# Kernel optimization log

Hardware: AMD Instinct MI355X
Metric: run time of the kernel (lower is better)

The kernel has to match this reference:

```python
import jax, jax.numpy as jnp
import numpy as np


def setup_inputs() -> dict:
    key = jax.random.key(0)
    ks = jax.random.split(key, 7)
    B, T, E, H = 4, 4096, 1024, 64
    return {
        "idx": jax.random.normal(ks[0], (B, T, E), dtype=jnp.float32),
        "Wq": jax.random.normal(ks[1], (E, H), dtype=jnp.float32) * (E ** -0.5),
        "bq": jax.random.normal(ks[2], (H,), dtype=jnp.float32) * 0.01,
        "Wk": jax.random.normal(ks[3], (E, H), dtype=jnp.float32) * (E ** -0.5),
        "bk": jax.random.normal(ks[4], (H,), dtype=jnp.float32) * 0.01,
        "Wv": jax.random.normal(ks[5], (E, H), dtype=jnp.float32) * (E ** -0.5),
        "bv": jax.random.normal(ks[6], (H,), dtype=jnp.float32) * 0.01,
    }


def reference(idx, Wq, bq, Wk, bk, Wv, bv):
    # idx: [B, T, E]
    d = idx.shape[-1]  # note: torch code scales by n_embd**-0.5, NOT head_size
    Q = idx @ Wq + bq  # [B, T, H]
    K = idx @ Wk + bk
    V = idx @ Wv + bv
    # scores; NOTE: original torch code calls wei.masked_fill(...) non-in-place
    # and discards the result, so no causal mask is applied. No softmax either.
    wei = jnp.einsum("bth,bsh->bts", Q, K) * (d ** -0.5)  # [B, T, T]
    out = jnp.einsum("bts,bsh->bth", wei, V)  # [B, T, H]
    return out
```

## Files before the change

### kernel.cpp

```cpp
#include <hip/hip_runtime.h>


typedef __attribute__((ext_vector_type(8))) short bf16x8;
typedef __attribute__((ext_vector_type(4))) float f32x4;

#define MFMA16(a, b, c) __builtin_amdgcn_mfma_f32_16x16x32_bf16((a), (b), (c), 0, 0, 0)

__device__ __forceinline__ unsigned short f2bf(float f) {
    unsigned int u = __float_as_uint(f);
    u += 0x7fffu + ((u >> 16) & 1u);
    return (unsigned short)(u >> 16);
}

__global__ void prep(const float* __restrict__ Wq, const float* __restrict__ Wk,
                     const float* __restrict__ Wv, unsigned short* __restrict__ WB,
                     float* __restrict__ Mf) {
    int t = blockIdx.x * 256 + threadIdx.x;
    if (t < 16384) Mf[t] = 0.f;
    int kki = t / 768;
    int rem = t - kki * 768;
    int nt = rem >> 6, lane = rem & 63;
    int n = nt * 16 + (lane & 15);
    int kb = kki * 32 + ((lane >> 4) * 8);
    int mm = n >> 6, h = n & 63;
    const float* W = (mm == 0) ? Wq : (mm == 1) ? Wk : Wv;
    float sc = (mm == 1) ? 0.03125f : 1.0f;
    bf16x8 v;
    #pragma unroll
    for (int j = 0; j < 8; j++) v[j] = (short)f2bf(W[(size_t)(kb + j) * 64 + h] * sc);
    *(bf16x8*)(WB + (size_t)t * 8) = v;
}

__global__ __launch_bounds__(256, 2) void qkv_m(
    const float* __restrict__ idx, const unsigned short* __restrict__ WB,
    const float* __restrict__ bq, const float* __restrict__ bk, const float* __restrict__ bv,
    unsigned short* __restrict__ Q, float* __restrict__ Mf) {
    __shared__ unsigned short As[32 * 1032];
    __shared__ unsigned short Lq[32 * 68];
    unsigned short* Lk = As;
    unsigned short* Lv = As + 64 * 36;

    const int tid = threadIdx.x, lane = tid & 63, w = tid >> 6;
    const int r0 = blockIdx.x * 32;

    {
        const float* src = idx + (size_t)(r0 + w * 8) * 1024;
        #pragma unroll
        for (int batch = 0; batch < 4; batch++) {
            float4 v[8];
            #pragma unroll
            for (int j = 0; j < 8; j++)
                v[j] = *(const float4*)(src + (size_t)(batch * 8 + j) * 256 + lane * 4);
            #pragma unroll
            for (int j = 0; j < 8; j++) {
                int i   = batch * 8 + j;
                int row = w * 8 + (i >> 2);
                int k   = (i & 3) * 256 + lane * 4;
                unsigned int lo = ((unsigned int)f2bf(v[j].y) << 16) | f2bf(v[j].x);
                unsigned int hi = ((unsigned int)f2bf(v[j].w) << 16) | f2bf(v[j].z);
                uint2 p; p.x = lo; p.y = hi;
                *(uint2*)(As + (size_t)row * 1032 + k) = p;
            }
        }
    }
    __syncthreads();

    const f32x4 z4 = {0.f, 0.f, 0.f, 0.f};
    f32x4 acc[2][3] = {{z4, z4, z4}, {z4, z4, z4}};
    {
        const unsigned short* a_base0 = As + (size_t)(lane & 15) * 1032 + ((lane >> 4) * 8);
        const unsigned short* a_base1 = a_base0 + 16 * 1032;
        bf16x8 a_c[2], b0[3], b1[3], b2[3];
        a_c[0] = *(const bf16x8*)a_base0;
        a_c[1] = *(const bf16x8*)a_base1;
        {
            const unsigned short* Bp0 = WB + (size_t)(lane * 8);
            const unsigned short* Bp1 = WB + (size_t)(12 * 64 + lane) * 8;
            #pragma unroll
            for (int j = 0; j < 3; j++) {
                b0[j] = *(const bf16x8*)(Bp0 + (w + j * 4) * 512);
                b1[j] = *(const bf16x8*)(Bp1 + (w + j * 4) * 512);
                b2[j] = b1[j];
            }
        }
        for (int kk = 0; kk < 32; kk++) {
            bf16x8 na0 = a_c[0], na1 = a_c[1];
            if (kk < 30) {
                const unsigned short* Bp = WB + (size_t)(((kk + 2) * 12) * 64 + lane) * 8;
                #pragma unroll
                for (int j = 0; j < 3; j++) b2[j] = *(const bf16x8*)(Bp + (w + j * 4) * 512);
            }
            if (kk < 31) {
                na0 = *(const bf16x8*)(a_base0 + (kk + 1) * 32);
                na1 = *(const bf16x8*)(a_base1 + (kk + 1) * 32);
            }
            #pragma unroll
            for (int j = 0; j < 3; j++) {
                acc[0][j] = MFMA16(a_c[0], b0[j], acc[0][j]);
                acc[1][j] = MFMA16(a_c[1], b0[j], acc[1][j]);
            }
            #pragma unroll
            for (int j = 0; j < 3; j++) { b0[j] = b1[j]; b1[j] = b2[j]; }
            a_c[0] = na0; a_c[1] = na1;
        }
    }

    __syncthreads();
    {
        const int h     = w * 16 + (lane & 15);
        const int rbase = (lane >> 4) * 4;
        float bias0 = bq[h], bias1 = bk[h] * 0.03125f, bias2 = bv[h];
        #pragma unroll
        for (int rf = 0; rf < 2; rf++) {
            #pragma unroll
            for (int reg = 0; reg < 4; reg++) {
                int r = rf * 16 + rbase + reg;
                Lq[r * 68 + h] = f2bf(acc[rf][0][reg] + bias0);
                Lk[h * 36 + r] = f2bf(acc[rf][1][reg] + bias1);
                Lv[h * 36 + r] = f2bf(acc[rf][2][reg] + bias2);
            }
        }
    }
    __syncthreads();

    {
        int qr = tid >> 3, qh = (tid & 7) * 8;
        *(uint4*)(Q + (size_t)(r0 + qr) * 64 + qh) = *(const uint4*)(Lq + qr * 68 + qh);
    }

    {
        const int tq = (lane >> 4) * 8;
        bf16x8 a = *(const bf16x8*)&Lk[(16 * w + (lane & 15)) * 36 + tq];
        f32x4 accM[4];
        #pragma unroll
        for (int nt = 0; nt < 4; nt++) {
            bf16x8 bb = *(const bf16x8*)&Lv[(nt * 16 + (lane & 15)) * 36 + tq];
            accM[nt] = MFMA16(a, bb, z4);
        }
        float* P = Mf + (size_t)(r0 >> 12) * 4096;
        const int rowb = 16 * w + (lane >> 4) * 4;
        #pragma unroll
        for (int nt = 0; nt < 4; nt++)
            #pragma unroll
            for (int reg = 0; reg < 4; reg++)
                atomicAdd(&P[(rowb + reg) * 64 + nt * 16 + (lane & 15)], accM[nt][reg]);
    }
}

__global__ __launch_bounds__(256) void qm(
    const unsigned short* __restrict__ Q, const float* __restrict__ Mf,
    float* __restrict__ out) {
    __shared__ unsigned short Lm[64 * 72];
    const int lane = threadIdx.x & 63, wave = threadIdx.x >> 6;
    const int r0 = blockIdx.x * 64;
    const int b  = r0 >> 12;
    {
        const int tt = threadIdx.x;
        int h1 = tt >> 2, h2c = (tt & 3) * 16;
        const float* Mp = Mf + (size_t)b * 4096 + h1 * 64 + h2c;
        float vals[16];
        *(float4*)(vals + 0)  = *(const float4*)(Mp + 0);
        *(float4*)(vals + 4)  = *(const float4*)(Mp + 4);
        *(float4*)(vals + 8)  = *(const float4*)(Mp + 8);
        *(float4*)(vals + 12) = *(const float4*)(Mp + 12);
        #pragma unroll
        for (int u = 0; u < 16; u++) Lm[(h2c + u) * 72 + h1] = f2bf(vals[u]);
    }
    __syncthreads();
    const f32x4 z4 = {0.f, 0.f, 0.f, 0.f};
    f32x4 acc[4] = {z4, z4, z4, z4};
    const int rr = r0 + 16 * wave + (lane & 15);
    const int kq = (lane >> 4) * 8;
    #pragma unroll
    for (int ks = 0; ks < 2; ks++) {
        int k0 = ks * 32;
        bf16x8 a = *(const bf16x8*)&Q[(size_t)rr * 64 + k0 + kq];
        #pragma unroll
        for (int nt = 0; nt < 4; nt++) {
            bf16x8 bb = *(const bf16x8*)&Lm[(size_t)(nt * 16 + (lane & 15)) * 72 + k0 + kq];
            acc[nt] = MFMA16(a, bb, acc[nt]);
        }
    }
    const int rowb = r0 + 16 * wave + (lane >> 4) * 4;
    #pragma unroll
    for (int nt = 0; nt < 4; nt++)
        #pragma unroll
        for (int reg = 0; reg < 4; reg++)
            out[(size_t)(rowb + reg) * 64 + nt * 16 + (lane & 15)] = acc[nt][reg];
}

extern "C" void kernel_launch(void* const* d_in, const int* in_sizes, int n_in,
                              void* d_out, int out_size, void* d_ws, size_t ws_size,
                              hipStream_t stream) {
    const float* idx = (const float*)d_in[0];
    const float* Wq  = (const float*)d_in[1];
    const float* bq  = (const float*)d_in[2];
    const float* Wk  = (const float*)d_in[3];
    const float* bk  = (const float*)d_in[4];
    const float* Wv  = (const float*)d_in[5];
    const float* bv  = (const float*)d_in[6];
    float* out = (float*)d_out;

    char* ws = (char*)d_ws;
    unsigned short* WB = (unsigned short*)(ws);
    float*          Mf = (float*)(ws + (1024u << 10));
    unsigned short* Q  = (unsigned short*)(ws + (2048u << 10));

    hipLaunchKernelGGL(prep,  dim3(96),  dim3(256), 0, stream, Wq, Wk, Wv, WB, Mf);
    hipLaunchKernelGGL(qkv_m, dim3(512), dim3(256), 0, stream,
                       idx, WB, bq, bk, bv, Q, Mf);
    hipLaunchKernelGGL(qm,    dim3(256), dim3(256), 0, stream, Q, Mf, out);
}
```

Before: 123.5 us.

## Stream A tiles straight from global and spread atomic reductions over partial buffers

The QKV projection kernel no longer stages the full 32x1024 input tile in shared memory. Each lane now loads its fp32 MFMA operand fragments directly from global memory, converts them with packed bf16 conversion instructions, and double-buffers them alongside the weight fragments. This frees about 66KB of LDS per block, so the launch bounds are raised to allow three blocks per CU. The K^T·V atomic accumulation is split across 8 partial copies chosen by block index to reduce contention on the same addresses, and the final kernel sums the 8 partials. The costs are that A loads are less coalesced, which relies on the cache, and the extra partial buffers must be zeroed and read.

```diff
diff --git a/kernel.cpp b/kernel.cpp
--- a/kernel.cpp
+++ b/kernel.cpp
@@ -12,11 +12,26 @@
     return (unsigned short)(u >> 16);
 }
 
+__device__ __forceinline__ unsigned int cvtpk(float a, float b) {
+    unsigned int r;
+    asm("v_cvt_pk_bf16_f32 %0, %1, %2" : "=v"(r) : "v"(a), "v"(b));
+    return r;
+}
+
+__device__ __forceinline__ bf16x8 cvt8(float4 lo, float4 hi) {
+    union { unsigned int u[4]; bf16x8 v; } r;
+    r.u[0] = cvtpk(lo.x, lo.y);
+    r.u[1] = cvtpk(lo.z, lo.w);
+    r.u[2] = cvtpk(hi.x, hi.y);
+    r.u[3] = cvtpk(hi.z, hi.w);
+    return r.v;
+}
+
 __global__ void prep(const float* __restrict__ Wq, const float* __restrict__ Wk,
                      const float* __restrict__ Wv, unsigned short* __restrict__ WB,
-                     float* __restrict__ Mf) {
+                     float* __restrict__ Mf8) {
     int t = blockIdx.x * 256 + threadIdx.x;
-    if (t < 16384) Mf[t] = 0.f;
+    for (int z = t; z < 131072; z += 24576) Mf8[z] = 0.f;
     int kki = t / 768;
     int rem = t - kki * 768;
     int nt = rem >> 6, lane = rem & 63;
@@ -31,81 +46,79 @@
     *(bf16x8*)(WB + (size_t)t * 8) = v;
 }
 
-__global__ __launch_bounds__(256, 2) void qkv_m(
+__global__ __launch_bounds__(256, 3) void qkv_m(
     const float* __restrict__ idx, const unsigned short* __restrict__ WB,
     const float* __restrict__ bq, const float* __restrict__ bk, const float* __restrict__ bv,
-    unsigned short* __restrict__ Q, float* __restrict__ Mf) {
-    __shared__ unsigned short As[32 * 1032];
+    unsigned short* __restrict__ Q, float* __restrict__ Mf8) {
     __shared__ unsigned short Lq[32 * 68];
-    unsigned short* Lk = As;
-    unsigned short* Lv = As + 64 * 36;
+    __shared__ unsigned short Lk[64 * 36];
+    __shared__ unsigned short Lv[64 * 36];
 
     const int tid = threadIdx.x, lane = tid & 63, w = tid >> 6;
     const int r0 = blockIdx.x * 32;
 
-    {
-        const float* src = idx + (size_t)(r0 + w * 8) * 1024;
-        #pragma unroll
-        for (int batch = 0; batch < 4; batch++) {
-            float4 v[8];
-            #pragma unroll
-            for (int j = 0; j < 8; j++)
-                v[j] = *(const float4*)(src + (size_t)(batch * 8 + j) * 256 + lane * 4);
-            #pragma unroll
-            for (int j = 0; j < 8; j++) {
-                int i   = batch * 8 + j;
-                int row = w * 8 + (i >> 2);
-                int k   = (i & 3) * 256 + lane * 4;
-                unsigned int lo = ((unsigned int)f2bf(v[j].y) << 16) | f2bf(v[j].x);
-                unsigned int hi = ((unsigned int)f2bf(v[j].w) << 16) | f2bf(v[j].z);
-                uint2 p; p.x = lo; p.y = hi;
-                *(uint2*)(As + (size_t)row * 1032 + k) = p;
-            }
-        }
-    }
-    __syncthreads();
+    const float* A0 = idx + (size_t)(r0 + (lane & 15)) * 1024 + ((lane >> 4) * 8);
+    const float* A1 = A0 + 16 * 1024;
+
+    float4 aA0 = *(const float4*)(A0 + 0),  aA1 = *(const float4*)(A0 + 4);
+    float4 aA2 = *(const float4*)(A1 + 0),  aA3 = *(const float4*)(A1 + 4);
+    float4 aB0 = *(const float4*)(A0 + 32), aB1 = *(const float4*)(A0 + 36);
+    float4 aB2 = *(const float4*)(A1 + 32), aB3 = *(const float4*)(A1 + 36);
+    bf16x8 bE[3], bO[3];
+    {
+        const unsigned short* Bp0 = WB + (size_t)(lane * 8);
+        const unsigned short* Bp1 = WB + (size_t)(12 * 64 + lane) * 8;
+        #pragma unroll
+        for (int j = 0; j < 3; j++) {
+            bE[j] = *(const bf16x8*)(Bp0 + (w + j * 4) * 512);
+            bO[j] = *(const bf16x8*)(Bp1 + (w + j * 4) * 512);
+        }
+    }
 
     const f32x4 z4 = {0.f, 0.f, 0.f, 0.f};
     f32x4 acc[2][3] = {{z4, z4, z4}, {z4, z4, z4}};
-    {
-        const unsigned short* a_base0 = As + (size_t)(lane & 15) * 1032 + ((lane >> 4) * 8);
-        const unsigned short* a_base1 = a_base0 + 16 * 1032;
-        bf16x8 a_c[2], b0[3], b1[3], b2[3];
-        a_c[0] = *(const bf16x8*)a_base0;
-        a_c[1] = *(const bf16x8*)a_base1;
+
+    for (int kk2 = 0; kk2 < 32; kk2 += 2) {
         {
-            const unsigned short* Bp0 = WB + (size_t)(lane * 8);
-            const unsigned short* Bp1 = WB + (size_t)(12 * 64 + lane) * 8;
-            #pragma unroll
-            for (int j = 0; j < 3; j++) {
-                b0[j] = *(const bf16x8*)(Bp0 + (w + j * 4) * 512);
-                b1[j] = *(const bf16x8*)(Bp1 + (w + j * 4) * 512);
-                b2[j] = b1[j];
-            }
-        }
-        for (int kk = 0; kk < 32; kk++) {
-            bf16x8 na0 = a_c[0], na1 = a_c[1];
-            if (kk < 30) {
-                const unsigned short* Bp = WB + (size_t)(((kk + 2) * 12) * 64 + lane) * 8;
+            bf16x8 a0 = cvt8(aA0, aA1), a1 = cvt8(aA2, aA3);
+            bf16x8 bu0 = bE[0], bu1 = bE[1], bu2 = bE[2];
+            if (kk2 < 30) {
+                const float* p0 = A0 + (kk2 + 2) * 32;
+                const float* p1 = A1 + (kk2 + 2) * 32;
+                aA0 = *(const float4*)p0; aA1 = *(const float4*)(p0 + 4);
+                aA2 = *(const float4*)p1; aA3 = *(const float4*)(p1 + 4);
+                const unsigned short* Bp = WB + (size_t)(((kk2 + 2) * 12) * 64 + lane) * 8;
                 #pragma unroll
-                for (int j = 0; j < 3; j++) b2[j] = *(const bf16x8*)(Bp + (w + j * 4) * 512);
-            }
-            if (kk < 31) {
-                na0 = *(const bf16x8*)(a_base0 + (kk + 1) * 32);
-                na1 = *(const bf16x8*)(a_base1 + (kk + 1) * 32);
-            }
-            #pragma unroll
-            for (int j = 0; j < 3; j++) {
-                acc[0][j] = MFMA16(a_c[0], b0[j], acc[0][j]);
-                acc[1][j] = MFMA16(a_c[1], b0[j], acc[1][j]);
-            }
-            #pragma unroll
-            for (int j = 0; j < 3; j++) { b0[j] = b1[j]; b1[j] = b2[j]; }
-            a_c[0] = na0; a_c[1] = na1;
-        }
-    }
-
-    __syncthreads();
+                for (int j = 0; j < 3; j++) bE[j] = *(const bf16x8*)(Bp + (w + j * 4) * 512);
+            }
+            acc[0][0] = MFMA16(a0, bu0, acc[0][0]);
+            acc[1][0] = MFMA16(a1, bu0, acc[1][0]);
+            acc[0][1] = MFMA16(a0, bu1, acc[0][1]);
+            acc[1][1] = MFMA16(a1, bu1, acc[1][1]);
+            acc[0][2] = MFMA16(a0, bu2, acc[0][2]);
+            acc[1][2] = MFMA16(a1, bu2, acc[1][2]);
+        }
+        {
+            bf16x8 a0 = cvt8(aB0, aB1), a1 = cvt8(aB2, aB3);
+            bf16x8 bu0 = bO[0], bu1 = bO[1], bu2 = bO[2];
+            if (kk2 < 30) {
+                const float* p0 = A0 + (kk2 + 3) * 32;
+                const float* p1 = A1 + (kk2 + 3) * 32;
+                aB0 = *(const float4*)p0; aB1 = *(const float4*)(p0 + 4);
+                aB2 = *(const float4*)p1; aB3 = *(const float4*)(p1 + 4);
+                const unsigned short* Bp = WB + (size_t)(((kk2 + 3) * 12) * 64 + lane) * 8;
+                #pragma unroll
+                for (int j = 0; j < 3; j++) bO[j] = *(const bf16x8*)(Bp + (w + j * 4) * 512);
+            }
+            acc[0][0] = MFMA16(a0, bu0, acc[0][0]);
+            acc[1][0] = MFMA16(a1, bu0, acc[1][0]);
+            acc[0][1] = MFMA16(a0, bu1, acc[0][1]);
+            acc[1][1] = MFMA16(a1, bu1, acc[1][1]);
+            acc[0][2] = MFMA16(a0, bu2, acc[0][2]);
+            acc[1][2] = MFMA16(a1, bu2, acc[1][2]);
+        }
+    }
+
     {
         const int h     = w * 16 + (lane & 15);
         const int rbase = (lane >> 4) * 4;
@@ -131,13 +144,14 @@
     {
         const int tq = (lane >> 4) * 8;
         bf16x8 a = *(const bf16x8*)&Lk[(16 * w + (lane & 15)) * 36 + tq];
+        const f32x4 z4b = {0.f, 0.f, 0.f, 0.f};
         f32x4 accM[4];
         #pragma unroll
         for (int nt = 0; nt < 4; nt++) {
             bf16x8 bb = *(const bf16x8*)&Lv[(nt * 16 + (lane & 15)) * 36 + tq];
-            accM[nt] = MFMA16(a, bb, z4);
-        }
-        float* P = Mf + (size_t)(r0 >> 12) * 4096;
+            accM[nt] = MFMA16(a, bb, z4b);
+        }
+        float* P = Mf8 + (((size_t)(blockIdx.x & 7) * 4) + (size_t)(r0 >> 12)) * 4096;
         const int rowb = 16 * w + (lane >> 4) * 4;
         #pragma unroll
         for (int nt = 0; nt < 4; nt++)
@@ -148,7 +162,7 @@
 }
 
 __global__ __launch_bounds__(256) void qm(
-    const unsigned short* __restrict__ Q, const float* __restrict__ Mf,
+    const unsigned short* __restrict__ Q, const float* __restrict__ Mf8,
     float* __restrict__ out) {
     __shared__ unsigned short Lm[64 * 72];
     const int lane = threadIdx.x & 63, wave = threadIdx.x >> 6;
@@ -157,12 +171,19 @@
     {
         const int tt = threadIdx.x;
         int h1 = tt >> 2, h2c = (tt & 3) * 16;
-        const float* Mp = Mf + (size_t)b * 4096 + h1 * 64 + h2c;
+        const float* Mp = Mf8 + (size_t)b * 4096 + h1 * 64 + h2c;
         float vals[16];
-        *(float4*)(vals + 0)  = *(const float4*)(Mp + 0);
-        *(float4*)(vals + 4)  = *(const float4*)(Mp + 4);
-        *(float4*)(vals + 8)  = *(const float4*)(Mp + 8);
-        *(float4*)(vals + 12) = *(const float4*)(Mp + 12);
+        #pragma unroll
+        for (int u = 0; u < 16; u += 4) *(float4*)(vals + u) = *(const float4*)(Mp + u);
+        #pragma unroll
+        for (int c = 1; c < 8; c++) {
+            const float* Mc = Mp + (size_t)c * 16384;
+            #pragma unroll
+            for (int u = 0; u < 16; u += 4) {
+                float4 t = *(const float4*)(Mc + u);
+                vals[u] += t.x; vals[u + 1] += t.y; vals[u + 2] += t.z; vals[u + 3] += t.w;
+            }
+        }
         #pragma unroll
         for (int u = 0; u < 16; u++) Lm[(h2c + u) * 72 + h1] = f2bf(vals[u]);
     }
@@ -202,12 +223,12 @@
     float* out = (float*)d_out;
 
     char* ws = (char*)d_ws;
-    unsigned short* WB = (unsigned short*)(ws);
-    float*          Mf = (float*)(ws + (1024u << 10));
-    unsigned short* Q  = (unsigned short*)(ws + (2048u << 10));
-
-    hipLaunchKernelGGL(prep,  dim3(96),  dim3(256), 0, stream, Wq, Wk, Wv, WB, Mf);
+    unsigned short* WB  = (unsigned short*)(ws);
+    float*          Mf8 = (float*)(ws + (1024u << 10));
+    unsigned short* Q   = (unsigned short*)(ws + (2048u << 10));
+
+    hipLaunchKernelGGL(prep,  dim3(96),  dim3(256), 0, stream, Wq, Wk, Wv, WB, Mf8);
     hipLaunchKernelGGL(qkv_m, dim3(512), dim3(256), 0, stream,
-                       idx, WB, bq, bk, bv, Q, Mf);
-    hipLaunchKernelGGL(qm,    dim3(256), dim3(256), 0, stream, Q, Mf, out);
-}
+                       idx, WB, bq, bk, bv, Q, Mf8);
+    hipLaunchKernelGGL(qm,    dim3(256), dim3(256), 0, stream, Q, Mf8, out);
+}
```

Result: slower. 138.5 us (+12.2%).

## Use 64-row tiles with 16 waves and replicated weight copies per block group

Applied to the files above, without the earlier changes.

Each qkv_m block now handles 64 rows with 1024 threads, and its 16 waves are split 4x4 over the 64 rows and 64 output column groups, so each wave keeps one row tile and three accumulators. The prep kernel writes four copies of the packed bf16 weights, and blocks pick a copy from their index to spread weight reads across different addresses and reduce contention. The K^T·V partial product now accumulates over 64 rows per block, which halves the number of atomicAdds into Mf. The cost is 132KB of LDS per block, which limits residency to one block per CU, and more workspace for the extra weight copies.

```diff
diff --git a/kernel.cpp b/kernel.cpp
--- a/kernel.cpp
+++ b/kernel.cpp
@@ -28,25 +28,25 @@
     bf16x8 v;
     #pragma unroll
     for (int j = 0; j < 8; j++) v[j] = (short)f2bf(W[(size_t)(kb + j) * 64 + h] * sc);
-    *(bf16x8*)(WB + (size_t)t * 8) = v;
-}
-
-__global__ __launch_bounds__(256, 2) void qkv_m(
+    #pragma unroll
+    for (int c = 0; c < 4; c++)
+        *(bf16x8*)(WB + (size_t)c * 196608 + (size_t)t * 8) = v;
+}
+
+__global__ __launch_bounds__(1024, 4) void qkv_m(
     const float* __restrict__ idx, const unsigned short* __restrict__ WB,
     const float* __restrict__ bq, const float* __restrict__ bk, const float* __restrict__ bv,
     unsigned short* __restrict__ Q, float* __restrict__ Mf) {
-    __shared__ unsigned short As[32 * 1032];
-    __shared__ unsigned short Lq[32 * 68];
-    unsigned short* Lk = As;
-    unsigned short* Lv = As + 64 * 36;
+    __shared__ unsigned short As[64 * 1032];
 
     const int tid = threadIdx.x, lane = tid & 63, w = tid >> 6;
-    const int r0 = blockIdx.x * 32;
-
-    {
-        const float* src = idx + (size_t)(r0 + w * 8) * 1024;
-        #pragma unroll
-        for (int batch = 0; batch < 4; batch++) {
+    const int wr = w >> 2, wc = w & 3;
+    const int r0 = blockIdx.x * 64;
+
+    {
+        const float* src = idx + (size_t)(r0 + w * 4) * 1024;
+        #pragma unroll
+        for (int batch = 0; batch < 2; batch++) {
             float4 v[8];
             #pragma unroll
             for (int j = 0; j < 8; j++)
@@ -54,7 +54,7 @@
             #pragma unroll
             for (int j = 0; j < 8; j++) {
                 int i   = batch * 8 + j;
-                int row = w * 8 + (i >> 2);
+                int row = w * 4 + (i >> 2);
                 int k   = (i & 3) * 256 + lane * 4;
                 unsigned int lo = ((unsigned int)f2bf(v[j].y) << 16) | f2bf(v[j].x);
                 unsigned int hi = ((unsigned int)f2bf(v[j].w) << 16) | f2bf(v[j].z);
@@ -66,84 +66,75 @@
     __syncthreads();
 
     const f32x4 z4 = {0.f, 0.f, 0.f, 0.f};
-    f32x4 acc[2][3] = {{z4, z4, z4}, {z4, z4, z4}};
-    {
-        const unsigned short* a_base0 = As + (size_t)(lane & 15) * 1032 + ((lane >> 4) * 8);
-        const unsigned short* a_base1 = a_base0 + 16 * 1032;
-        bf16x8 a_c[2], b0[3], b1[3], b2[3];
-        a_c[0] = *(const bf16x8*)a_base0;
-        a_c[1] = *(const bf16x8*)a_base1;
+    f32x4 acc[3] = {z4, z4, z4};
+    {
+        const unsigned short* WBc = WB + (size_t)((blockIdx.x >> 3) & 3) * 196608;
+        const unsigned short* a_base =
+            As + (size_t)(wr * 16 + (lane & 15)) * 1032 + ((lane >> 4) * 8);
+        bf16x8 a_c = *(const bf16x8*)a_base;
+        bf16x8 b0[3], b1[3], b2[3];
         {
-            const unsigned short* Bp0 = WB + (size_t)(lane * 8);
-            const unsigned short* Bp1 = WB + (size_t)(12 * 64 + lane) * 8;
+            const unsigned short* Bp0 = WBc + (size_t)(lane * 8);
+            const unsigned short* Bp1 = WBc + (size_t)(12 * 64 + lane) * 8;
             #pragma unroll
             for (int j = 0; j < 3; j++) {
-                b0[j] = *(const bf16x8*)(Bp0 + (w + j * 4) * 512);
-                b1[j] = *(const bf16x8*)(Bp1 + (w + j * 4) * 512);
+                b0[j] = *(const bf16x8*)(Bp0 + (wc + j * 4) * 512);
+                b1[j] = *(const bf16x8*)(Bp1 + (wc + j * 4) * 512);
                 b2[j] = b1[j];
             }
         }
         for (int kk = 0; kk < 32; kk++) {
-            bf16x8 na0 = a_c[0], na1 = a_c[1];
+            bf16x8 na = a_c;
             if (kk < 30) {
-                const unsigned short* Bp = WB + (size_t)(((kk + 2) * 12) * 64 + lane) * 8;
+                const unsigned short* Bp = WBc + (size_t)(((kk + 2) * 12) * 64 + lane) * 8;
                 #pragma unroll
-                for (int j = 0; j < 3; j++) b2[j] = *(const bf16x8*)(Bp + (w + j * 4) * 512);
+                for (int j = 0; j < 3; j++) b2[j] = *(const bf16x8*)(Bp + (wc + j * 4) * 512);
             }
-            if (kk < 31) {
-                na0 = *(const bf16x8*)(a_base0 + (kk + 1) * 32);
-                na1 = *(const bf16x8*)(a_base1 + (kk + 1) * 32);
-            }
-            #pragma unroll
-            for (int j = 0; j < 3; j++) {
-                acc[0][j] = MFMA16(a_c[0], b0[j], acc[0][j]);
-                acc[1][j] = MFMA16(a_c[1], b0[j], acc[1][j]);
-            }
+            if (kk < 31) na = *(const bf16x8*)(a_base + (kk + 1) * 32);
+            #pragma unroll
+            for (int j = 0; j < 3; j++) acc[j] = MFMA16(a_c, b0[j], acc[j]);
             #pragma unroll
             for (int j = 0; j < 3; j++) { b0[j] = b1[j]; b1[j] = b2[j]; }
-            a_c[0] = na0; a_c[1] = na1;
-        }
-    }
-
-    __syncthreads();
-    {
-        const int h     = w * 16 + (lane & 15);
-        const int rbase = (lane >> 4) * 4;
-        float bias0 = bq[h], bias1 = bk[h] * 0.03125f, bias2 = bv[h];
-        #pragma unroll
-        for (int rf = 0; rf < 2; rf++) {
-            #pragma unroll
-            for (int reg = 0; reg < 4; reg++) {
-                int r = rf * 16 + rbase + reg;
-                Lq[r * 68 + h] = f2bf(acc[rf][0][reg] + bias0);
-                Lk[h * 36 + r] = f2bf(acc[rf][1][reg] + bias1);
-                Lv[h * 36 + r] = f2bf(acc[rf][2][reg] + bias2);
-            }
-        }
-    }
-    __syncthreads();
-
-    {
-        int qr = tid >> 3, qh = (tid & 7) * 8;
-        *(uint4*)(Q + (size_t)(r0 + qr) * 64 + qh) = *(const uint4*)(Lq + qr * 68 + qh);
-    }
-
-    {
-        const int tq = (lane >> 4) * 8;
-        bf16x8 a = *(const bf16x8*)&Lk[(16 * w + (lane & 15)) * 36 + tq];
-        f32x4 accM[4];
-        #pragma unroll
-        for (int nt = 0; nt < 4; nt++) {
-            bf16x8 bb = *(const bf16x8*)&Lv[(nt * 16 + (lane & 15)) * 36 + tq];
-            accM[nt] = MFMA16(a, bb, z4);
+            a_c = na;
+        }
+    }
+
+    __syncthreads();
+    unsigned short* Lq = As;
+    unsigned short* Lk = As + 4608;
+    unsigned short* Lv = As + 9216;
+    {
+        const int col   = wc * 16 + (lane & 15);
+        const int rbase = wr * 16 + (lane >> 4) * 4;
+        float b0v = bq[col], b1v = bk[col] * 0.03125f, b2v = bv[col];
+        #pragma unroll
+        for (int reg = 0; reg < 4; reg++) {
+            int r = rbase + reg;
+            Lq[r * 72 + col] = f2bf(acc[0][reg] + b0v);
+            Lk[col * 72 + r] = f2bf(acc[1][reg] + b1v);
+            Lv[col * 72 + r] = f2bf(acc[2][reg] + b2v);
+        }
+    }
+    __syncthreads();
+
+    {
+        int row = tid >> 4, c4 = (tid & 15) * 4;
+        *(uint2*)(Q + (size_t)(r0 + row) * 64 + c4) = *(const uint2*)(Lq + row * 72 + c4);
+    }
+
+    {
+        f32x4 accM = z4;
+        #pragma unroll
+        for (int ts = 0; ts < 64; ts += 32) {
+            bf16x8 ka = *(const bf16x8*)(Lk + (wr * 16 + (lane & 15)) * 72 + ts + (lane >> 4) * 8);
+            bf16x8 vb = *(const bf16x8*)(Lv + (wc * 16 + (lane & 15)) * 72 + ts + (lane >> 4) * 8);
+            accM = MFMA16(ka, vb, accM);
         }
         float* P = Mf + (size_t)(r0 >> 12) * 4096;
-        const int rowb = 16 * w + (lane >> 4) * 4;
-        #pragma unroll
-        for (int nt = 0; nt < 4; nt++)
-            #pragma unroll
-            for (int reg = 0; reg < 4; reg++)
-                atomicAdd(&P[(rowb + reg) * 64 + nt * 16 + (lane & 15)], accM[nt][reg]);
+        const int rowb = wr * 16 + (lane >> 4) * 4;
+        #pragma unroll
+        for (int reg = 0; reg < 4; reg++)
+            atomicAdd(&P[(rowb + reg) * 64 + wc * 16 + (lane & 15)], accM[reg]);
     }
 }
 
@@ -203,11 +194,11 @@
 
     char* ws = (char*)d_ws;
     unsigned short* WB = (unsigned short*)(ws);
-    float*          Mf = (float*)(ws + (1024u << 10));
-    unsigned short* Q  = (unsigned short*)(ws + (2048u << 10));
-
-    hipLaunchKernelGGL(prep,  dim3(96),  dim3(256), 0, stream, Wq, Wk, Wv, WB, Mf);
-    hipLaunchKernelGGL(qkv_m, dim3(512), dim3(256), 0, stream,
+    float*          Mf = (float*)(ws + (2048u << 10));
+    unsigned short* Q  = (unsigned short*)(ws + (3072u << 10));
+
+    hipLaunchKernelGGL(prep,  dim3(96),  dim3(256),  0, stream, Wq, Wk, Wv, WB, Mf);
+    hipLaunchKernelGGL(qkv_m, dim3(256), dim3(1024), 0, stream,
                        idx, WB, bq, bk, bv, Q, Mf);
-    hipLaunchKernelGGL(qm,    dim3(256), dim3(256), 0, stream, Q, Mf, out);
-}
+    hipLaunchKernelGGL(qm,    dim3(256), dim3(256),  0, stream, Q, Mf, out);
+}
```

Measured after the change: 123.4 us. About the same (-0.0%).
